# Kernel optimization log

Measured on AMD Instinct MI355X. Metric: run time of the kernel, lower is better.

Reference implementation:

```python
import jax, jax.numpy as jnp
import numpy as np

DIM = 1024
N_HEADS = 16
HEAD_DIM = DIM // N_HEADS  # 64
B, T = 4, 2048


def setup_inputs() -> dict:
    key = jax.random.key(0)
    ks = jax.random.split(key, 6)
    x = jax.random.normal(ks[0], (B, T, DIM), dtype=jnp.float32)
    # causal mask; original does att.masked_fill(mask == 0, -inf)
    mask = jnp.tril(jnp.ones((T, T), dtype=bool))[None, None, :, :]
    s = 1.0 / np.sqrt(DIM)
    Wq = jax.random.normal(ks[1], (DIM, DIM), dtype=jnp.float32) * s
    Wk = jax.random.normal(ks[2], (DIM, DIM), dtype=jnp.float32) * s
    Wv = jax.random.normal(ks[3], (DIM, DIM), dtype=jnp.float32) * s
    Wo = jax.random.normal(ks[4], (DIM, DIM), dtype=jnp.float32) * s
    bo = jnp.zeros((DIM,), dtype=jnp.float32)
    return {"x": x, "mask": mask, "Wq": Wq, "Wk": Wk, "Wv": Wv,
            "Wo": Wo, "bo": bo, "start_pos": 0}


def reference(x, mask, Wq, Wk, Wv, Wo, bo, start_pos):
    Bx, Tx, C = x.shape
    # torch nn.Linear: y = x @ W.T (no bias for QKV)
    q = jnp.einsum('btc,dc->btd', x, Wq).reshape(Bx, Tx, N_HEADS, HEAD_DIM)
    k = jnp.einsum('btc,dc->btd', x, Wk).reshape(Bx, Tx, N_HEADS, HEAD_DIM)
    v = jnp.einsum('btc,dc->btd', x, Wv).reshape(Bx, Tx, N_HEADS, HEAD_DIM)
    # no caching path: keys=k, values=v
    scale = 1.0 / jnp.sqrt(jnp.asarray(HEAD_DIM, dtype=x.dtype))
    # [B, H, Tq, Tk]
    att = jnp.einsum('bqhd,bkhd->bhqk', q, k) * scale
    att = jnp.where(mask, att, jnp.asarray(-jnp.inf, dtype=att.dtype))
    att = jax.nn.softmax(att, axis=-1)
    out = jnp.einsum('bhqk,bkhd->bqhd', att, v).reshape(Bx, Tx, C)
    return jnp.einsum('btc,dc->btd', out, Wo) + bo
```

## Files before the change

### kernel.cpp

```cpp
#include <hip/hip_runtime.h>
#include <cstdint>
#include <cstddef>

typedef __bf16 bf16;
typedef bf16 bf16x8 __attribute__((ext_vector_type(8)));
typedef float f32x4 __attribute__((ext_vector_type(4)));
typedef float f32x16 __attribute__((ext_vector_type(16)));

__device__ inline f32x4 mfma_16x16x32(bf16x8 a, bf16x8 b, f32x4 c) {
    return __builtin_amdgcn_mfma_f32_16x16x32_bf16(a, b, c, 0, 0, 0);
}
__device__ inline f32x16 mfma_32x32x16(bf16x8 a, bf16x8 b, f32x16 c) {
    return __builtin_amdgcn_mfma_f32_32x32x16_bf16(a, b, c, 0, 0, 0);
}
__device__ inline uint32_t cvt_pk_bf16(float lo, float hi) {
    uint32_t r;
    asm("v_cvt_pk_bf16_f32 %0, %1, %2" : "=v"(r) : "v"(lo), "v"(hi));
    return r;
}

#define GLD16(gsrc, ldst)                                                              \
    __builtin_amdgcn_global_load_lds(                                                  \
        (const __attribute__((address_space(1))) uint32_t*)(gsrc),                     \
        (__attribute__((address_space(3))) uint32_t*)(ldst), 16, 0, 0)

__global__ void cvt_kernel(const float* __restrict__ src, bf16* __restrict__ dst, int n) {
    int i = (blockIdx.x * blockDim.x + threadIdx.x) * 4;
    if (i >= n) return;
    float4 f = *(const float4*)(src + i);
    union { bf16 o4[4]; uint2 u; } pk;
    pk.o4[0] = (bf16)f.x; pk.o4[1] = (bf16)f.y; pk.o4[2] = (bf16)f.z; pk.o4[3] = (bf16)f.w;
    *(uint2*)(dst + i) = pk.u;
}

__global__ void cvt4_kernel(const float* __restrict__ s0, const float* __restrict__ s1,
                            const float* __restrict__ s2, const float* __restrict__ s3,
                            bf16* __restrict__ d0, bf16* __restrict__ d1,
                            bf16* __restrict__ d2, bf16* __restrict__ d3) {
    const int z = blockIdx.y;
    const float* src = (z == 0) ? s0 : (z == 1) ? s1 : (z == 2) ? s2 : s3;
    bf16* dst = (z == 0) ? d0 : (z == 1) ? d1 : (z == 2) ? d2 : d3;
    int i = (blockIdx.x * blockDim.x + threadIdx.x) * 4;
    float4 f = *(const float4*)(src + i);
    union { bf16 o4[4]; uint2 u; } pk;
    pk.o4[0] = (bf16)f.x; pk.o4[1] = (bf16)f.y; pk.o4[2] = (bf16)f.z; pk.o4[3] = (bf16)f.w;
    *(uint2*)(dst + i) = pk.u;
}

#define BM 128
#define BN 128
#define BK 64
#define QSCALE 0.18033688011112042f

__global__ __launch_bounds__(256, 2)
void gemm_qkv(const bf16* __restrict__ xb,
              const bf16* __restrict__ wq, const bf16* __restrict__ wk, const bf16* __restrict__ wv,
              bf16* __restrict__ qo, bf16* __restrict__ ko, bf16* __restrict__ vo)
{
    __shared__ bf16 sA[BM][BK];
    __shared__ bf16 sB[BN][BK];
    const int K = 1024;
    const int tid = threadIdx.x;
    const int lane = tid & 63, wave = tid >> 6;
    const int wm = wave >> 1, wn = wave & 1;
    const int quad = lane >> 4, ln = lane & 15;
    const int lr = lane >> 3;
    const int ssc = ((lane & 7) ^ lr) * 8;
    const int lnm = ln & 7;
    const int rc0 = (quad ^ lnm) * 8;
    const int rc1 = ((4 | quad) ^ lnm) * 8;
    const int id = blockIdx.x;
    const int z = id >> 9;
    const int xt = (id & 511) >> 6;
    const int yt = id & 63;
    const bf16* W = (z == 0) ? wq : (z == 1) ? wk : wv;
    const int row0 = yt * BM;
    const int col0 = xt * BN;

    f32x4 acc[4][4];
    const f32x4 zero = {0.f, 0.f, 0.f, 0.f};
#pragma unroll
    for (int i = 0; i < 4; ++i)
#pragma unroll
        for (int j = 0; j < 4; ++j) acc[i][j] = zero;

    for (int k0 = 0; k0 < K; k0 += BK) {
#pragma unroll
        for (int s = 0; s < 4; ++s) {
            int ra = wave * 32 + s * 8;
            GLD16(&xb[(size_t)(row0 + ra + lr) * K + k0 + ssc], &sA[ra][0]);
            GLD16(&W [(size_t)(col0 + ra + lr) * K + k0 + ssc], &sB[ra][0]);
        }
        __syncthreads();
#pragma unroll
        for (int kk = 0; kk < BK; kk += 32) {
            const int rc = kk ? rc1 : rc0;
            bf16x8 af[4], bfv[4];
#pragma unroll
            for (int i = 0; i < 4; ++i) {
                af[i]  = *(const bf16x8*)(&sA[wm * 64 + i * 16 + ln][rc]);
                bfv[i] = *(const bf16x8*)(&sB[wn * 64 + i * 16 + ln][rc]);
            }
#pragma unroll
            for (int mi = 0; mi < 4; ++mi)
#pragma unroll
                for (int ni = 0; ni < 4; ++ni)
                    acc[mi][ni] = mfma_16x16x32(af[mi], bfv[ni], acc[mi][ni]);
        }
        __syncthreads();
    }
    if (z == 2) {
#pragma unroll
        for (int mi = 0; mi < 4; ++mi)
#pragma unroll
            for (int ni = 0; ni < 4; ++ni) {
                int gm0 = row0 + wm * 64 + mi * 16 + quad * 4;
                int gn = col0 + wn * 64 + ni * 16 + ln;
                int b = gm0 >> 11, t = gm0 & 2047;
                int h = gn >> 6,  d = gn & 63;
                union { bf16 v[4]; uint2 u; } pk;
#pragma unroll
                for (int i = 0; i < 4; ++i) pk.v[i] = (bf16)acc[mi][ni][i];
                *(uint2*)(&vo[((size_t)((b * 16 + h) * 64 + d)) * 2048 + t]) = pk.u;
            }
    } else {
        const float scale = (z == 0) ? QSCALE : 1.0f;
        bf16* outp = (z == 0) ? qo : ko;
#pragma unroll
        for (int mi = 0; mi < 4; ++mi)
#pragma unroll
            for (int ni = 0; ni < 4; ++ni)
#pragma unroll
                for (int i = 0; i < 4; ++i) {
                    int gm = row0 + wm * 64 + mi * 16 + quad * 4 + i;
                    int gn = col0 + wn * 64 + ni * 16 + ln;
                    int b = gm >> 11, t = gm & 2047;
                    int h = gn >> 6,  d = gn & 63;
                    outp[((size_t)((b * 16 + h) * 2048 + t)) * 64 + d] = (bf16)(acc[mi][ni][i] * scale);
                }
    }
}

__global__ __launch_bounds__(256, 2)
void gemm_out(const bf16* __restrict__ ab, const bf16* __restrict__ wo,
              const float* __restrict__ bias, float* __restrict__ out)
{
    __shared__ bf16 sA[BM][BK];
    __shared__ bf16 sB[BN][BK];
    const int K = 1024;
    const int tid = threadIdx.x;
    const int lane = tid & 63, wave = tid >> 6;
    const int wm = wave >> 1, wn = wave & 1;
    const int quad = lane >> 4, ln = lane & 15;
    const int lr = lane >> 3;
    const int ssc = ((lane & 7) ^ lr) * 8;
    const int lnm = ln & 7;
    const int rc0 = (quad ^ lnm) * 8;
    const int rc1 = ((4 | quad) ^ lnm) * 8;
    const int id = blockIdx.x;
    const int xt = id >> 6, yt = id & 63;
    const int row0 = yt * BM;
    const int col0 = xt * BN;

    f32x4 acc[4][4];
    const f32x4 zero = {0.f, 0.f, 0.f, 0.f};
#pragma unroll
    for (int i = 0; i < 4; ++i)
#pragma unroll
        for (int j = 0; j < 4; ++j) acc[i][j] = zero;

    for (int k0 = 0; k0 < K; k0 += BK) {
#pragma unroll
        for (int s = 0; s < 4; ++s) {
            int ra = wave * 32 + s * 8;
            GLD16(&ab[(size_t)(row0 + ra + lr) * K + k0 + ssc], &sA[ra][0]);
            GLD16(&wo[(size_t)(col0 + ra + lr) * K + k0 + ssc], &sB[ra][0]);
        }
        __syncthreads();
#pragma unroll
        for (int kk = 0; kk < BK; kk += 32) {
            const int rc = kk ? rc1 : rc0;
            bf16x8 af[4], bfv[4];
#pragma unroll
            for (int i = 0; i < 4; ++i) {
                af[i]  = *(const bf16x8*)(&sA[wm * 64 + i * 16 + ln][rc]);
                bfv[i] = *(const bf16x8*)(&sB[wn * 64 + i * 16 + ln][rc]);
            }
#pragma unroll
            for (int mi = 0; mi < 4; ++mi)
#pragma unroll
                for (int ni = 0; ni < 4; ++ni)
                    acc[mi][ni] = mfma_16x16x32(af[mi], bfv[ni], acc[mi][ni]);
        }
        __syncthreads();
    }
#pragma unroll
    for (int mi = 0; mi < 4; ++mi)
#pragma unroll
        for (int ni = 0; ni < 4; ++ni)
#pragma unroll
            for (int i = 0; i < 4; ++i) {
                int gm = row0 + wm * 64 + mi * 16 + quad * 4 + i;
                int gn = col0 + wn * 64 + ni * 16 + ln;
                out[(size_t)gm * 1024 + gn] = acc[mi][ni][i] + bias[gn];
            }
}

__global__ __launch_bounds__(256, 2)
void flash_attn(const bf16* __restrict__ q, const bf16* __restrict__ k,
                const bf16* __restrict__ vt, bf16* __restrict__ ao)
{
    __shared__ bf16 sK[64][72];
    __shared__ bf16 sV[64][72];
    const int tid = threadIdx.x, lane = tid & 63, w = tid >> 6;
    const int c31 = lane & 31, hi = lane >> 5, hi8 = hi * 8;
    const int id = blockIdx.x;
    const int bh = id & 63;
    const int q0 = (15 - (id >> 6)) * 128;
    const size_t base = (size_t)bh * (2048 * 64);
    const int sr = tid >> 3, sc = (tid & 7) * 8;
    const int rw = q0 + w * 32;
    const int rw31 = rw + 31;
    const int qrow = rw + c31;

    bf16x8 qf[4];
#pragma unroll
    for (int dt = 0; dt < 4; ++dt)
        qf[dt] = *(const bf16x8*)(&q[base + (size_t)qrow * 64 + dt * 16 + hi8]);

    const f32x16 z16 = {0.f,0.f,0.f,0.f,0.f,0.f,0.f,0.f,0.f,0.f,0.f,0.f,0.f,0.f,0.f,0.f};
    f32x16 o0 = z16, o1 = z16;
    float lsum = 0.f;

    const int kend = q0 + 128;
    uint4 rKa = *(const uint4*)(&k [base + (size_t)sr * 64 + sc]);
    uint4 rKb = *(const uint4*)(&k [base + (size_t)(sr + 32) * 64 + sc]);
    uint4 rVa = *(const uint4*)(&vt[base + (size_t)sr * 2048 + sc]);
    uint4 rVb = *(const uint4*)(&vt[base + (size_t)(sr + 32) * 2048 + sc]);

    for (int k0 = 0; k0 < kend; k0 += 64) {
        __syncthreads();
        *(uint4*)(&sK[sr][sc])      = rKa;
        *(uint4*)(&sK[sr + 32][sc]) = rKb;
        *(uint4*)(&sV[sr][sc])      = rVa;
        *(uint4*)(&sV[sr + 32][sc]) = rVb;
        __syncthreads();
        if (k0 + 64 < kend) {
            int kn = k0 + 64;
            rKa = *(const uint4*)(&k [base + (size_t)(kn + sr) * 64 + sc]);
            rKb = *(const uint4*)(&k [base + (size_t)(kn + sr + 32) * 64 + sc]);
            rVa = *(const uint4*)(&vt[base + (size_t)sr * 2048 + kn + sc]);
            rVb = *(const uint4*)(&vt[base + (size_t)(sr + 32) * 2048 + kn + sc]);
        }
        if (k0 <= rw31) {
#pragma unroll
            for (int kt = 0; kt < 2; ++kt) {
                const int ktb = k0 + kt * 32;
                if (ktb <= rw31) {
                    bf16x8 kf0 = *(const bf16x8*)(&sK[kt * 32 + c31][ 0 + hi8]);
                    bf16x8 kf1 = *(const bf16x8*)(&sK[kt * 32 + c31][16 + hi8]);
                    bf16x8 kf2 = *(const bf16x8*)(&sK[kt * 32 + c31][32 + hi8]);
                    bf16x8 kf3 = *(const bf16x8*)(&sK[kt * 32 + c31][48 + hi8]);
                    f32x16 st = z16;
                    st = mfma_32x32x16(kf0, qf[0], st);
                    st = mfma_32x32x16(kf1, qf[1], st);
                    st = mfma_32x32x16(kf2, qf[2], st);
                    st = mfma_32x32x16(kf3, qf[3], st);
                    const int kb2 = ktb + hi * 4;
                    if (ktb + 31 > rw) {
#pragma unroll
                        for (int r = 0; r < 16; ++r) {
                            int kk = kb2 + (r & 3) + 8 * (r >> 2);
                            if (kk > qrow) st[r] = -INFINITY;
                        }
                    }
                    float pp[16];
                    float ps = 0.f;
#pragma unroll
                    for (int r = 0; r < 16; ++r) {
                        float p = __builtin_amdgcn_exp2f(st[r]);
                        ps += p;
                        pp[r] = p;
                    }
                    lsum += ps;
#pragma unroll
                    for (int ks = 0; ks < 2; ++ks) {
                        const int ob = ks * 8;
                        uint32_t a0 = cvt_pk_bf16(pp[ob + 0], pp[ob + 1]);
                        uint32_t a1 = cvt_pk_bf16(pp[ob + 2], pp[ob + 3]);
                        uint32_t a2 = cvt_pk_bf16(pp[ob + 4], pp[ob + 5]);
                        uint32_t a3 = cvt_pk_bf16(pp[ob + 6], pp[ob + 7]);
                        auto r02 = __builtin_amdgcn_permlane32_swap(a0, a2, false, false);
                        auto r13 = __builtin_amdgcn_permlane32_swap(a1, a3, false, false);
                        union { uint32_t u[4]; bf16x8 v; } af;
                        af.u[0] = r02[0]; af.u[1] = r13[0];
                        af.u[2] = r02[1]; af.u[3] = r13[1];
                        const int co = kt * 32 + ks * 16 + hi8;
                        bf16x8 v0 = *(const bf16x8*)(&sV[c31][co]);
                        bf16x8 v1 = *(const bf16x8*)(&sV[32 + c31][co]);
                        o0 = mfma_32x32x16(v0, af.v, o0);
                        o1 = mfma_32x32x16(v1, af.v, o1);
                    }
                }
            }
        }
    }

    float l = lsum + __shfl_xor(lsum, 32);
    const float inv = 1.0f / l;
    const int b = bh >> 4, h = bh & 15;
    bf16* orow = &ao[(size_t)(b * 2048 + qrow) * 1024 + h * 64];
#pragma unroll
    for (int g = 0; g < 4; ++g) {
        union { bf16 v4[4]; uint2 u; } pk0, pk1;
#pragma unroll
        for (int i = 0; i < 4; ++i) {
            pk0.v4[i] = (bf16)(o0[g * 4 + i] * inv);
            pk1.v4[i] = (bf16)(o1[g * 4 + i] * inv);
        }
        *(uint2*)(&orow[     g * 8 + hi * 4]) = pk0.u;
        *(uint2*)(&orow[32 + g * 8 + hi * 4]) = pk1.u;
    }
}

extern "C" void kernel_launch(void* const* d_in, const int* in_sizes, int n_in,
                              void* d_out, int out_size, void* d_ws, size_t ws_size,
                              hipStream_t stream) {
    const float* x  = (const float*)d_in[0];
    const float* Wq = (const float*)d_in[2];
    const float* Wk = (const float*)d_in[3];
    const float* Wv = (const float*)d_in[4];
    const float* Wo = (const float*)d_in[5];
    const float* bo = (const float*)d_in[6];
    float* out = (float*)d_out;

    char* p = (char*)d_ws;
    const size_t MK = 8192ull * 1024;
    bf16* xb  = (bf16*)p; p += MK * 2;
    bf16* wqb = (bf16*)p; p += (1ull << 20) * 2;
    bf16* wkb = (bf16*)p; p += (1ull << 20) * 2;
    bf16* wvb = (bf16*)p; p += (1ull << 20) * 2;
    bf16* wob = (bf16*)p; p += (1ull << 20) * 2;
    bf16* qb  = (bf16*)p; p += MK * 2;
    bf16* kb  = (bf16*)p; p += MK * 2;
    bf16* vtb = (bf16*)p; p += MK * 2;
    bf16* aob = (bf16*)p; p += MK * 2;

    cvt_kernel<<<(int)(MK / 1024), 256, 0, stream>>>(x, xb, (int)MK);
    cvt4_kernel<<<dim3(1024, 4), 256, 0, stream>>>(Wq, Wk, Wv, Wo, wqb, wkb, wvb, wob);

    gemm_qkv<<<1536, 256, 0, stream>>>(xb, wqb, wkb, wvb, qb, kb, vtb);
    flash_attn<<<1024, 256, 0, stream>>>(qb, kb, vtb, aob);
    gemm_out<<<512, 256, 0, stream>>>(aob, wob, bo, out);
}
```

Before: 230.5 us.

## Double-buffer GEMM LDS with 256x128 tiles and 8-wave interleaved schedule

Rewrites the QKV and output projection GEMMs to use 512-thread blocks on 256x128 tiles with double-buffered dynamic LDS. Global-to-LDS loads for tile k+2 are issued while the current tile's MFMAs run, with split MFMA phases, s_setprio and explicit vmcnt waits. This is meant to hide load latency and cut barrier stalls from the old single-buffer loop. In exchange it uses 96KB LDS with one block per CU and fewer blocks in total, which lowers occupancy.

```diff
diff --git a/kernel.cpp b/kernel.cpp
--- a/kernel.cpp
+++ b/kernel.cpp
@@ -47,68 +47,154 @@
     *(uint2*)(dst + i) = pk.u;
 }
 
-#define BM 128
-#define BN 128
 #define BK 64
 #define QSCALE 0.18033688011112042f
 
-__global__ __launch_bounds__(256, 2)
+#define GEMM_PRELUDE                                                          \
+    extern __shared__ char smem[];                                            \
+    bf16 (*sA)[256][64] = (bf16 (*)[256][64])smem;                            \
+    bf16 (*sB)[128][64] = (bf16 (*)[128][64])(smem + 2 * 256 * 64 * 2);       \
+    const int tid = threadIdx.x;                                              \
+    const int lane = tid & 63, wave = tid >> 6;                               \
+    const int wm = wave >> 1, wn = wave & 1;                                  \
+    const int quad = lane >> 4, ln = lane & 15;                               \
+    const int lr = lane >> 3;                                                 \
+    const int ssc = ((lane & 7) ^ lr) * 8;                                    \
+    const int lnm = ln & 7;                                                   \
+    const int rc0 = (quad ^ lnm) * 8;                                         \
+    const int rc1 = ((4 | quad) ^ lnm) * 8;                                   \
+    const int wmr = wm * 64, wnr = wn * 64;                                   \
+    const int ra0 = wave * 16, ra1 = wave * 16 + 8;                           \
+    const int ra2 = 128 + wave * 16, ra3 = 136 + wave * 16;                   \
+    const int rb0 = wave * 8, rb1 = 64 + wave * 8;
+
+#define STAGEA(tn) do { const int cb_ = (tn) & 1; const size_t ko_ = (size_t)(tn) * 64; \
+    GLD16(aSrc0 + ko_, &sA[cb_][ra0][0]);                                     \
+    GLD16(aSrc1 + ko_, &sA[cb_][ra1][0]);                                     \
+    GLD16(aSrc2 + ko_, &sA[cb_][ra2][0]);                                     \
+    GLD16(aSrc3 + ko_, &sA[cb_][ra3][0]); } while (0)
+#define STAGEB(tn) do { const int cb_ = (tn) & 1; const size_t ko_ = (size_t)(tn) * 64; \
+    GLD16(bSrc0 + ko_, &sB[cb_][rb0][0]);                                     \
+    GLD16(bSrc1 + ko_, &sB[cb_][rb1][0]); } while (0)
+
+#define LGKM0_FENCE                                                           \
+    asm volatile("s_waitcnt lgkmcnt(0)" ::: "memory");                        \
+    __builtin_amdgcn_sched_barrier(0);
+
+#define ITER(T, DOSTAGE, EVM) do {                                            \
+    const int cur_ = (T) & 1;                                                 \
+    bf16x8 a0_[2][2], b0_[2][2], a1_[2][2], b1_[2][2];                        \
+                                                  \
+    _Pragma("unroll")                                                         \
+    for (int mi = 0; mi < 2; ++mi) {                                          \
+        a0_[mi][0] = *(const bf16x8*)(&sA[cur_][wmr + mi * 16 + ln][rc0]);    \
+        a0_[mi][1] = *(const bf16x8*)(&sA[cur_][wmr + mi * 16 + ln][rc1]);    \
+        b0_[mi][0] = *(const bf16x8*)(&sB[cur_][wnr + mi * 16 + ln][rc0]);    \
+        b0_[mi][1] = *(const bf16x8*)(&sB[cur_][wnr + mi * 16 + ln][rc1]);    \
+    }                                                                         \
+    __builtin_amdgcn_s_barrier();                                             \
+    LGKM0_FENCE                                                               \
+    __builtin_amdgcn_s_setprio(1);                                            \
+    _Pragma("unroll")                                                         \
+    for (int mi = 0; mi < 2; ++mi)                                            \
+        _Pragma("unroll")                                                     \
+        for (int ni = 0; ni < 2; ++ni) {                                      \
+            acc[mi][ni] = mfma_16x16x32(a0_[mi][0], b0_[ni][0], acc[mi][ni]); \
+            acc[mi][ni] = mfma_16x16x32(a0_[mi][1], b0_[ni][1], acc[mi][ni]); \
+        }                                                                     \
+    __builtin_amdgcn_s_setprio(0);                                            \
+    __builtin_amdgcn_s_barrier();                                             \
+                                                  \
+    _Pragma("unroll")                                                         \
+    for (int mi = 0; mi < 2; ++mi) {                                          \
+        a1_[mi][0] = *(const bf16x8*)(&sA[cur_][wmr + 32 + mi * 16 + ln][rc0]); \
+        a1_[mi][1] = *(const bf16x8*)(&sA[cur_][wmr + 32 + mi * 16 + ln][rc1]); \
+    }                                                                         \
+    __builtin_amdgcn_s_barrier();                                             \
+    LGKM0_FENCE                                                               \
+    __builtin_amdgcn_s_setprio(1);                                            \
+    _Pragma("unroll")                                                         \
+    for (int mi = 0; mi < 2; ++mi)                                            \
+        _Pragma("unroll")                                                     \
+        for (int ni = 0; ni < 2; ++ni) {                                      \
+            acc[2 + mi][ni] = mfma_16x16x32(a1_[mi][0], b0_[ni][0], acc[2 + mi][ni]); \
+            acc[2 + mi][ni] = mfma_16x16x32(a1_[mi][1], b0_[ni][1], acc[2 + mi][ni]); \
+        }                                                                     \
+    __builtin_amdgcn_s_setprio(0);                                            \
+    __builtin_amdgcn_s_barrier();                                             \
+        \
+    _Pragma("unroll")                                                         \
+    for (int ni = 0; ni < 2; ++ni) {                                          \
+        b1_[ni][0] = *(const bf16x8*)(&sB[cur_][wnr + 32 + ni * 16 + ln][rc0]); \
+        b1_[ni][1] = *(const bf16x8*)(&sB[cur_][wnr + 32 + ni * 16 + ln][rc1]); \
+    }                                                                         \
+    if (DOSTAGE) { STAGEA((T) + 2); }                                         \
+    __builtin_amdgcn_s_barrier();                                             \
+    LGKM0_FENCE                                                               \
+    __builtin_amdgcn_s_setprio(1);                                            \
+    _Pragma("unroll")                                                         \
+    for (int mi = 0; mi < 2; ++mi)                                            \
+        _Pragma("unroll")                                                     \
+        for (int ni = 0; ni < 2; ++ni) {                                      \
+            acc[2 + mi][2 + ni] = mfma_16x16x32(a1_[mi][0], b1_[ni][0], acc[2 + mi][2 + ni]); \
+            acc[2 + mi][2 + ni] = mfma_16x16x32(a1_[mi][1], b1_[ni][1], acc[2 + mi][2 + ni]); \
+        }                                                                     \
+    __builtin_amdgcn_s_setprio(0);                                            \
+    __builtin_amdgcn_s_barrier();                                             \
+     \
+    if (DOSTAGE) { STAGEB((T) + 2); }                                         \
+    __builtin_amdgcn_s_barrier();                                             \
+    __builtin_amdgcn_s_setprio(1);                                            \
+    _Pragma("unroll")                                                         \
+    for (int mi = 0; mi < 2; ++mi)                                            \
+        _Pragma("unroll")                                                     \
+        for (int ni = 0; ni < 2; ++ni) {                                      \
+            acc[mi][2 + ni] = mfma_16x16x32(a0_[mi][0], b1_[ni][0], acc[mi][2 + ni]); \
+            acc[mi][2 + ni] = mfma_16x16x32(a0_[mi][1], b1_[ni][1], acc[mi][2 + ni]); \
+        }                                                                     \
+    __builtin_amdgcn_s_setprio(0);                                            \
+    if ((EVM) == 6)      asm volatile("s_waitcnt vmcnt(6)" ::: "memory");     \
+    else if ((EVM) == 0) asm volatile("s_waitcnt vmcnt(0)" ::: "memory");     \
+    __builtin_amdgcn_s_barrier();                                             \
+} while (0)
+
+#define GEMM_MAINLOOP                                                         \
+    f32x4 acc[4][4];                                                          \
+    const f32x4 zero = {0.f, 0.f, 0.f, 0.f};                                  \
+    _Pragma("unroll")                                                         \
+    for (int i = 0; i < 4; ++i)                                               \
+        _Pragma("unroll")                                                     \
+        for (int j = 0; j < 4; ++j) acc[i][j] = zero;                         \
+    STAGEA(0); STAGEB(0); STAGEA(1); STAGEB(1);                               \
+    asm volatile("s_waitcnt vmcnt(6)" ::: "memory");                          \
+    __builtin_amdgcn_s_barrier();                                             \
+    _Pragma("unroll 2")                                                       \
+    for (int t = 0; t < 14; ++t) { ITER(t, 1, 6); }                           \
+    ITER(14, 0, 0);                                                           \
+    ITER(15, 0, -1);
+
+__global__ __launch_bounds__(512, 1)
 void gemm_qkv(const bf16* __restrict__ xb,
               const bf16* __restrict__ wq, const bf16* __restrict__ wk, const bf16* __restrict__ wv,
               bf16* __restrict__ qo, bf16* __restrict__ ko, bf16* __restrict__ vo)
 {
-    __shared__ bf16 sA[BM][BK];
-    __shared__ bf16 sB[BN][BK];
-    const int K = 1024;
-    const int tid = threadIdx.x;
-    const int lane = tid & 63, wave = tid >> 6;
-    const int wm = wave >> 1, wn = wave & 1;
-    const int quad = lane >> 4, ln = lane & 15;
-    const int lr = lane >> 3;
-    const int ssc = ((lane & 7) ^ lr) * 8;
-    const int lnm = ln & 7;
-    const int rc0 = (quad ^ lnm) * 8;
-    const int rc1 = ((4 | quad) ^ lnm) * 8;
+    GEMM_PRELUDE
     const int id = blockIdx.x;
-    const int z = id >> 9;
-    const int xt = (id & 511) >> 6;
-    const int yt = id & 63;
+    const int z = id >> 8;
+    const int xt = (id >> 5) & 7;
+    const int yt = id & 31;
     const bf16* W = (z == 0) ? wq : (z == 1) ? wk : wv;
-    const int row0 = yt * BM;
-    const int col0 = xt * BN;
-
-    f32x4 acc[4][4];
-    const f32x4 zero = {0.f, 0.f, 0.f, 0.f};
-#pragma unroll
-    for (int i = 0; i < 4; ++i)
-#pragma unroll
-        for (int j = 0; j < 4; ++j) acc[i][j] = zero;
-
-    for (int k0 = 0; k0 < K; k0 += BK) {
-#pragma unroll
-        for (int s = 0; s < 4; ++s) {
-            int ra = wave * 32 + s * 8;
-            GLD16(&xb[(size_t)(row0 + ra + lr) * K + k0 + ssc], &sA[ra][0]);
-            GLD16(&W [(size_t)(col0 + ra + lr) * K + k0 + ssc], &sB[ra][0]);
-        }
-        __syncthreads();
-#pragma unroll
-        for (int kk = 0; kk < BK; kk += 32) {
-            const int rc = kk ? rc1 : rc0;
-            bf16x8 af[4], bfv[4];
-#pragma unroll
-            for (int i = 0; i < 4; ++i) {
-                af[i]  = *(const bf16x8*)(&sA[wm * 64 + i * 16 + ln][rc]);
-                bfv[i] = *(const bf16x8*)(&sB[wn * 64 + i * 16 + ln][rc]);
-            }
-#pragma unroll
-            for (int mi = 0; mi < 4; ++mi)
-#pragma unroll
-                for (int ni = 0; ni < 4; ++ni)
-                    acc[mi][ni] = mfma_16x16x32(af[mi], bfv[ni], acc[mi][ni]);
-        }
-        __syncthreads();
-    }
+    const int row0 = yt * 256;
+    const int col0 = xt * 128;
+    const bf16* aSrc0 = xb + (size_t)(row0 + ra0 + lr) * 1024 + ssc;
+    const bf16* aSrc1 = xb + (size_t)(row0 + ra1 + lr) * 1024 + ssc;
+    const bf16* aSrc2 = xb + (size_t)(row0 + ra2 + lr) * 1024 + ssc;
+    const bf16* aSrc3 = xb + (size_t)(row0 + ra3 + lr) * 1024 + ssc;
+    const bf16* bSrc0 = W  + (size_t)(col0 + rb0 + lr) * 1024 + ssc;
+    const bf16* bSrc1 = W  + (size_t)(col0 + rb1 + lr) * 1024 + ssc;
+
+    GEMM_MAINLOOP
+
     if (z == 2) {
 #pragma unroll
         for (int mi = 0; mi < 4; ++mi)
@@ -141,59 +227,24 @@
     }
 }
 
-__global__ __launch_bounds__(256, 2)
+__global__ __launch_bounds__(512, 1)
 void gemm_out(const bf16* __restrict__ ab, const bf16* __restrict__ wo,
               const float* __restrict__ bias, float* __restrict__ out)
 {
-    __shared__ bf16 sA[BM][BK];
-    __shared__ bf16 sB[BN][BK];
-    const int K = 1024;
-    const int tid = threadIdx.x;
-    const int lane = tid & 63, wave = tid >> 6;
-    const int wm = wave >> 1, wn = wave & 1;
-    const int quad = lane >> 4, ln = lane & 15;
-    const int lr = lane >> 3;
-    const int ssc = ((lane & 7) ^ lr) * 8;
-    const int lnm = ln & 7;
-    const int rc0 = (quad ^ lnm) * 8;
-    const int rc1 = ((4 | quad) ^ lnm) * 8;
+    GEMM_PRELUDE
     const int id = blockIdx.x;
-    const int xt = id >> 6, yt = id & 63;
-    const int row0 = yt * BM;
-    const int col0 = xt * BN;
-
-    f32x4 acc[4][4];
-    const f32x4 zero = {0.f, 0.f, 0.f, 0.f};
-#pragma unroll
-    for (int i = 0; i < 4; ++i)
-#pragma unroll
-        for (int j = 0; j < 4; ++j) acc[i][j] = zero;
-
-    for (int k0 = 0; k0 < K; k0 += BK) {
-#pragma unroll
-        for (int s = 0; s < 4; ++s) {
-            int ra = wave * 32 + s * 8;
-            GLD16(&ab[(size_t)(row0 + ra + lr) * K + k0 + ssc], &sA[ra][0]);
-            GLD16(&wo[(size_t)(col0 + ra + lr) * K + k0 + ssc], &sB[ra][0]);
-        }
-        __syncthreads();
-#pragma unroll
-        for (int kk = 0; kk < BK; kk += 32) {
-            const int rc = kk ? rc1 : rc0;
-            bf16x8 af[4], bfv[4];
-#pragma unroll
-            for (int i = 0; i < 4; ++i) {
-                af[i]  = *(const bf16x8*)(&sA[wm * 64 + i * 16 + ln][rc]);
-                bfv[i] = *(const bf16x8*)(&sB[wn * 64 + i * 16 + ln][rc]);
-            }
-#pragma unroll
-            for (int mi = 0; mi < 4; ++mi)
-#pragma unroll
-                for (int ni = 0; ni < 4; ++ni)
-                    acc[mi][ni] = mfma_16x16x32(af[mi], bfv[ni], acc[mi][ni]);
-        }
-        __syncthreads();
-    }
+    const int xt = id >> 5, yt = id & 31;
+    const int row0 = yt * 256;
+    const int col0 = xt * 128;
+    const bf16* aSrc0 = ab + (size_t)(row0 + ra0 + lr) * 1024 + ssc;
+    const bf16* aSrc1 = ab + (size_t)(row0 + ra1 + lr) * 1024 + ssc;
+    const bf16* aSrc2 = ab + (size_t)(row0 + ra2 + lr) * 1024 + ssc;
+    const bf16* aSrc3 = ab + (size_t)(row0 + ra3 + lr) * 1024 + ssc;
+    const bf16* bSrc0 = wo + (size_t)(col0 + rb0 + lr) * 1024 + ssc;
+    const bf16* bSrc1 = wo + (size_t)(col0 + rb1 + lr) * 1024 + ssc;
+
+    GEMM_MAINLOOP
+
 #pragma unroll
     for (int mi = 0; mi < 4; ++mi)
 #pragma unroll
@@ -346,10 +397,19 @@
     bf16* vtb = (bf16*)p; p += MK * 2;
     bf16* aob = (bf16*)p; p += MK * 2;
 
+    static bool attr_done = false;
+    if (!attr_done) {
+        hipFuncSetAttribute(reinterpret_cast<const void*>(&gemm_qkv),
+                            hipFuncAttributeMaxDynamicSharedMemorySize, 98304);
+        hipFuncSetAttribute(reinterpret_cast<const void*>(&gemm_out),
+                            hipFuncAttributeMaxDynamicSharedMemorySize, 98304);
+        attr_done = true;
+    }
+
     cvt_kernel<<<(int)(MK / 1024), 256, 0, stream>>>(x, xb, (int)MK);
     cvt4_kernel<<<dim3(1024, 4), 256, 0, stream>>>(Wq, Wk, Wv, Wo, wqb, wkb, wvb, wob);
 
-    gemm_qkv<<<1536, 256, 0, stream>>>(xb, wqb, wkb, wvb, qb, kb, vtb);
+    gemm_qkv<<<768, 512, 98304, stream>>>(xb, wqb, wkb, wvb, qb, kb, vtb);
     flash_attn<<<1024, 256, 0, stream>>>(qb, kb, vtb, aob);
-    gemm_out<<<512, 256, 0, stream>>>(aob, wob, bo, out);
-}
+    gemm_out<<<256, 512, 98304, stream>>>(aob, wob, bo, out);
+}
```

Measured after the change: 236.1 us. 2.4% more time.

## Double-buffer K/V LDS tiles in attention and merge conversion kernels

Applied to the files above, without the earlier changes.

The flash attention kernel now keeps two LDS buffers for K and V. The next tile is written into the alternate buffer after the current tile's compute, so each iteration needs one barrier instead of two. MFMA sections are wrapped in s_setprio to favour matrix issue across waves. The two fp32-to-bf16 conversion launches are merged into a single kernel to save one launch. LDS use doubles, which may affect occupancy at two blocks per CU.

```diff
diff --git a/kernel.cpp b/kernel.cpp
--- a/kernel.cpp
+++ b/kernel.cpp
@@ -24,23 +24,26 @@
         (const __attribute__((address_space(1))) uint32_t*)(gsrc),                     \
         (__attribute__((address_space(3))) uint32_t*)(ldst), 16, 0, 0)
 
-__global__ void cvt_kernel(const float* __restrict__ src, bf16* __restrict__ dst, int n) {
-    int i = (blockIdx.x * blockDim.x + threadIdx.x) * 4;
-    if (i >= n) return;
-    float4 f = *(const float4*)(src + i);
-    union { bf16 o4[4]; uint2 u; } pk;
-    pk.o4[0] = (bf16)f.x; pk.o4[1] = (bf16)f.y; pk.o4[2] = (bf16)f.z; pk.o4[3] = (bf16)f.w;
-    *(uint2*)(dst + i) = pk.u;
-}
-
-__global__ void cvt4_kernel(const float* __restrict__ s0, const float* __restrict__ s1,
-                            const float* __restrict__ s2, const float* __restrict__ s3,
-                            bf16* __restrict__ d0, bf16* __restrict__ d1,
-                            bf16* __restrict__ d2, bf16* __restrict__ d3) {
-    const int z = blockIdx.y;
-    const float* src = (z == 0) ? s0 : (z == 1) ? s1 : (z == 2) ? s2 : s3;
-    bf16* dst = (z == 0) ? d0 : (z == 1) ? d1 : (z == 2) ? d2 : d3;
-    int i = (blockIdx.x * blockDim.x + threadIdx.x) * 4;
+__global__ void cvt_all(const float* __restrict__ x,
+                        const float* __restrict__ w0, const float* __restrict__ w1,
+                        const float* __restrict__ w2, const float* __restrict__ w3,
+                        bf16* __restrict__ xb,
+                        bf16* __restrict__ d0, bf16* __restrict__ d1,
+                        bf16* __restrict__ d2, bf16* __restrict__ d3) {
+    const int id = blockIdx.x;
+    const float* src;
+    bf16* dst;
+    int boff;
+    if (id < 8192) {
+        src = x; dst = xb; boff = id;
+    } else {
+        const int r = id - 8192;
+        const int z = r >> 10;
+        boff = r & 1023;
+        src = (z == 0) ? w0 : (z == 1) ? w1 : (z == 2) ? w2 : w3;
+        dst = (z == 0) ? d0 : (z == 1) ? d1 : (z == 2) ? d2 : d3;
+    }
+    const size_t i = ((size_t)boff * 256 + threadIdx.x) * 4;
     float4 f = *(const float4*)(src + i);
     union { bf16 o4[4]; uint2 u; } pk;
     pk.o4[0] = (bf16)f.x; pk.o4[1] = (bf16)f.y; pk.o4[2] = (bf16)f.z; pk.o4[3] = (bf16)f.w;
@@ -210,8 +213,8 @@
 void flash_attn(const bf16* __restrict__ q, const bf16* __restrict__ k,
                 const bf16* __restrict__ vt, bf16* __restrict__ ao)
 {
-    __shared__ bf16 sK[64][72];
-    __shared__ bf16 sV[64][72];
+    __shared__ bf16 sK[2][64][72];
+    __shared__ bf16 sV[2][64][72];
     const int tid = threadIdx.x, lane = tid & 63, w = tid >> 6;
     const int c31 = lane & 31, hi = lane >> 5, hi8 = hi * 8;
     const int id = blockIdx.x;
@@ -232,21 +235,22 @@
     f32x16 o0 = z16, o1 = z16;
     float lsum = 0.f;
 
-    const int kend = q0 + 128;
+    const int nt = (q0 >> 6) + 2;
     uint4 rKa = *(const uint4*)(&k [base + (size_t)sr * 64 + sc]);
     uint4 rKb = *(const uint4*)(&k [base + (size_t)(sr + 32) * 64 + sc]);
     uint4 rVa = *(const uint4*)(&vt[base + (size_t)sr * 2048 + sc]);
     uint4 rVb = *(const uint4*)(&vt[base + (size_t)(sr + 32) * 2048 + sc]);
-
-    for (int k0 = 0; k0 < kend; k0 += 64) {
-        __syncthreads();
-        *(uint4*)(&sK[sr][sc])      = rKa;
-        *(uint4*)(&sK[sr + 32][sc]) = rKb;
-        *(uint4*)(&sV[sr][sc])      = rVa;
-        *(uint4*)(&sV[sr + 32][sc]) = rVb;
-        __syncthreads();
-        if (k0 + 64 < kend) {
-            int kn = k0 + 64;
+    *(uint4*)(&sK[0][sr][sc])      = rKa;
+    *(uint4*)(&sK[0][sr + 32][sc]) = rKb;
+    *(uint4*)(&sV[0][sr][sc])      = rVa;
+    *(uint4*)(&sV[0][sr + 32][sc]) = rVb;
+    __syncthreads();
+
+    for (int t = 0; t < nt; ++t) {
+        const int cur = t & 1;
+        const int k0 = t * 64;
+        if (t + 1 < nt) {
+            const int kn = k0 + 64;
             rKa = *(const uint4*)(&k [base + (size_t)(kn + sr) * 64 + sc]);
             rKb = *(const uint4*)(&k [base + (size_t)(kn + sr + 32) * 64 + sc]);
             rVa = *(const uint4*)(&vt[base + (size_t)sr * 2048 + kn + sc]);
@@ -257,15 +261,17 @@
             for (int kt = 0; kt < 2; ++kt) {
                 const int ktb = k0 + kt * 32;
                 if (ktb <= rw31) {
-                    bf16x8 kf0 = *(const bf16x8*)(&sK[kt * 32 + c31][ 0 + hi8]);
-                    bf16x8 kf1 = *(const bf16x8*)(&sK[kt * 32 + c31][16 + hi8]);
-                    bf16x8 kf2 = *(const bf16x8*)(&sK[kt * 32 + c31][32 + hi8]);
-                    bf16x8 kf3 = *(const bf16x8*)(&sK[kt * 32 + c31][48 + hi8]);
+                    bf16x8 kf0 = *(const bf16x8*)(&sK[cur][kt * 32 + c31][ 0 + hi8]);
+                    bf16x8 kf1 = *(const bf16x8*)(&sK[cur][kt * 32 + c31][16 + hi8]);
+                    bf16x8 kf2 = *(const bf16x8*)(&sK[cur][kt * 32 + c31][32 + hi8]);
+                    bf16x8 kf3 = *(const bf16x8*)(&sK[cur][kt * 32 + c31][48 + hi8]);
                     f32x16 st = z16;
+                    __builtin_amdgcn_s_setprio(1);
                     st = mfma_32x32x16(kf0, qf[0], st);
                     st = mfma_32x32x16(kf1, qf[1], st);
                     st = mfma_32x32x16(kf2, qf[2], st);
                     st = mfma_32x32x16(kf3, qf[3], st);
+                    __builtin_amdgcn_s_setprio(0);
                     const int kb2 = ktb + hi * 4;
                     if (ktb + 31 > rw) {
 #pragma unroll
@@ -296,14 +302,23 @@
                         af.u[0] = r02[0]; af.u[1] = r13[0];
                         af.u[2] = r02[1]; af.u[3] = r13[1];
                         const int co = kt * 32 + ks * 16 + hi8;
-                        bf16x8 v0 = *(const bf16x8*)(&sV[c31][co]);
-                        bf16x8 v1 = *(const bf16x8*)(&sV[32 + c31][co]);
+                        bf16x8 v0 = *(const bf16x8*)(&sV[cur][c31][co]);
+                        bf16x8 v1 = *(const bf16x8*)(&sV[cur][32 + c31][co]);
+                        __builtin_amdgcn_s_setprio(1);
                         o0 = mfma_32x32x16(v0, af.v, o0);
                         o1 = mfma_32x32x16(v1, af.v, o1);
+                        __builtin_amdgcn_s_setprio(0);
                     }
                 }
             }
         }
+        if (t + 1 < nt) {
+            *(uint4*)(&sK[cur ^ 1][sr][sc])      = rKa;
+            *(uint4*)(&sK[cur ^ 1][sr + 32][sc]) = rKb;
+            *(uint4*)(&sV[cur ^ 1][sr][sc])      = rVa;
+            *(uint4*)(&sV[cur ^ 1][sr + 32][sc]) = rVb;
+        }
+        __syncthreads();
     }
 
     float l = lsum + __shfl_xor(lsum, 32);
@@ -346,8 +361,7 @@
     bf16* vtb = (bf16*)p; p += MK * 2;
     bf16* aob = (bf16*)p; p += MK * 2;
 
-    cvt_kernel<<<(int)(MK / 1024), 256, 0, stream>>>(x, xb, (int)MK);
-    cvt4_kernel<<<dim3(1024, 4), 256, 0, stream>>>(Wq, Wk, Wv, Wo, wqb, wkb, wvb, wob);
+    cvt_all<<<12288, 256, 0, stream>>>(x, Wq, Wk, Wv, Wo, xb, wqb, wkb, wvb, wob);
 
     gemm_qkv<<<1536, 256, 0, stream>>>(xb, wqb, wkb, wvb, qb, kb, vtb);
     flash_attn<<<1024, 256, 0, stream>>>(qb, kb, vtb, aob);
```

Result: no change. 230.9 us (+0.1%).
